# Kernel optimization log

Measured on AMD Instinct MI355X. Metric: run time of the kernel, lower is better.

The kernel has to match this reference:

```python
import jax, jax.numpy as jnp
import numpy as np


def pairwise_distance(x):
    # x: [B,N,F] -> squared euclidean distance matrix [B,N,N]
    sq = jnp.sum(x * x, axis=-1)
    d = sq[:, :, None] + sq[:, None, :] - 2.0 * jnp.einsum('bnd,bmd->bnm', x, x)
    return jnp.maximum(d, 0.0)


def knn_adjacency(dist, k):
    # keep the k nearest neighbors of each point (binary adjacency)
    B, N, _ = dist.shape
    idx = jax.lax.top_k(-dist, k)[1]  # [B,N,k]
    A = jnp.zeros((B, N, N), dist.dtype)
    return A.at[jnp.arange(B)[:, None, None], jnp.arange(N)[None, :, None], idx].set(1.0)


def get_laplacian(A):
    # normalized graph Laplacian L = I - D^{-1/2} A D^{-1/2}
    d = jnp.sum(A, axis=-1)
    dinv = jnp.where(d > 0, 1.0 / jnp.sqrt(jnp.maximum(d, 1e-12)), 0.0)
    An = A * dinv[:, :, None] * dinv[:, None, :]
    return jnp.eye(A.shape[-1], dtype=A.dtype)[None] - An


def cheb_conv(x, L, W, b, K):
    # DenseChebConv: Chebyshev recurrence T0=x, T1=Lx, Tk=2L T_{k-1}-T_{k-2};
    # concat along features then dense projection. x:[B,N,Fin], W:[K*Fin,Fout]
    xs = [x]
    if K > 1:
        xs.append(jnp.einsum('bnm,bmf->bnf', L, x))
    for _ in range(2, K):
        xs.append(2.0 * jnp.einsum('bnm,bmf->bnf', L, xs[-1]) - xs[-2])
    xk = jnp.concatenate(xs, axis=-1)
    return jnp.einsum('bnf,fo->bno', xk, W) + b


def segment_max(out, idx):
    # fused replacement of the per-batch/per-cluster python loops:
    # out:[B,N,F], idx:[B,R,S] -> max-pooled cluster features [B,R,F]
    B = out.shape[0]
    g = out[jnp.arange(B)[:, None, None], idx]  # [B,R,S,F]
    return jnp.max(g, axis=2)


def setup_inputs():
    key = jax.random.key(0)
    ks = jax.random.split(key, 12)
    B, N, R, S, P = 32, 1024, 64, 16, 55
    inp = {}
    inp['x'] = jax.random.normal(ks[0], (B, N, 7), jnp.float32)
    inp['x2'] = jax.random.normal(ks[1], (B, N, 3), jnp.float32)
    inp['laplacian_Reeb'] = jax.random.normal(ks[2], (B, R, R), jnp.float32)
    inp['W1'] = jax.random.normal(ks[3], (3 * 7, 64), jnp.float32) * 0.1
    inp['b1'] = jnp.zeros((64,), jnp.float32)
    inp['W_reeb'] = jax.random.normal(ks[4], (6 * 64, 256), jnp.float32) * 0.05
    inp['b_reeb'] = jnp.zeros((256,), jnp.float32)
    inp['W_fps'] = jax.random.normal(ks[5], (6 * 64, 256), jnp.float32) * 0.05
    inp['b_fps'] = jnp.zeros((256,), jnp.float32)
    inp['fc1_w'] = jax.random.normal(ks[6], (512, 256), jnp.float32) * 0.05
    inp['fc1_b'] = jnp.zeros((256,), jnp.float32)
    inp['fc3_w'] = jax.random.normal(ks[7], (256, 40), jnp.float32) * 0.05
    inp['fc3_b'] = jnp.zeros((40,), jnp.float32)
    inp['sccs'] = jax.random.randint(ks[8], (B, R, S), 0, N)
    inp['sccs_fps'] = jax.random.randint(ks[9], (B, P, N), 0, N)
    inp['k'] = 30
    inp['batch_size'] = B
    inp['num_points'] = N
    return inp


def reference(x, x2, laplacian_Reeb, W1, b1, W_reeb, b_reeb, W_fps, b_fps,
              fc1_w, fc1_b, fc3_w, fc3_b, sccs, sccs_fps, k, batch_size, num_points):
    sg = jax.lax.stop_gradient
    # point-cloud kNN Laplacian (torch.no_grad in original)
    L = sg(get_laplacian(knn_adjacency(pairwise_distance(x), k)))
    out = jax.nn.relu(cheb_conv(x, L, W1, b1, 3))  # [B,N,64]
    reg1 = jnp.sum(jnp.einsum('bnf,bnm,bmg->bfg', out, L, out) ** 2)
    # Reeb-graph segment max pooling (no_grad in original)
    V_reeb = sg(segment_max(out, sccs))  # [B,R,64]
    L_reeb = sg(laplacian_Reeb)
    out_reeb = jax.nn.relu(cheb_conv(V_reeb, L_reeb, W_reeb, b_reeb, 6))  # [B,R,256]
    reg2 = jnp.sum(jnp.einsum('bnf,bnm,bmg->bfg', out_reeb, L_reeb, out_reeb) ** 2)
    # FPS cluster max pooling (no_grad in original)
    V_fps = sg(segment_max(out, sccs_fps))  # [B,55,64]
    L_fps = sg(get_laplacian(pairwise_distance(V_fps)))
    out_fps = jax.nn.relu(cheb_conv(V_fps, L_fps, W_fps, b_fps, 6))  # [B,55,256]
    reg3 = jnp.sum(jnp.einsum('bnf,bnm,bmg->bfg', out_fps, L_fps, out_fps) ** 2)
    feat = jnp.concatenate([jnp.max(out_reeb, axis=1), jnp.max(out_fps, axis=1)], axis=1)  # [B,512]
    h = jax.nn.relu(feat @ fc1_w + fc1_b)
    logits = h @ fc3_w + fc3_b  # [B,40]
    regs = jnp.stack([reg1, reg2, reg3,
                      jnp.sum(fc1_w[:, 0] ** 2), fc1_b[0] ** 2,
                      jnp.sum(fc3_w[:, 0] ** 2), fc3_b[0] ** 2])
    return logits, regs
```

## Files before the change

### kernel.cpp

```cpp
#include <hip/hip_runtime.h>
#include <math.h>

#define BN 32
#define NP 1024
#define KNN 30
#define NR 64
#define NFPS 55

#define XSLOT(r) ((r) * 8 + ((r) >> 7) * 4)

__device__ __forceinline__ float lap_s() {
    const float dv = 1.0f / sqrtf(30.0f);
    return dv * dv;
}

__device__ __forceinline__ float dist7(const float4& xiA, const float4& xiB,
                                       float sqi, const float4& ca, const float4& cb) {
#pragma clang fp contract(off)
    float dot = xiA.x * ca.x;
    dot = fmaf(xiA.y, ca.y, dot);
    dot = fmaf(xiA.z, ca.z, dot);
    dot = fmaf(xiA.w, ca.w, dot);
    dot = fmaf(xiB.x, cb.x, dot);
    dot = fmaf(xiB.y, cb.y, dot);
    dot = fmaf(xiB.z, cb.z, dot);
    float r = sqi + cb.w;
    r = r - 2.f * dot;
    return fmaxf(r, 0.f);
}

__global__ __launch_bounds__(256, 4) void k_knn(const float* __restrict__ x,
                                                int* __restrict__ knn,
                                                float* __restrict__ xs1) {
    __shared__ float xls[8224];
    int b = blockIdx.x;
    int t = threadIdx.x;
    int ln = t & 63, wv = t >> 6;
    int seg = ln & 7;
    int rl  = ln >> 3;

    const float* xb = x + (size_t)b * NP * 7;
#pragma unroll 4
    for (int k = 0; k < 32; ++k) {
        int q = k * 256 + t;
        int r = q >> 3, d = q & 7;
        float v = (d < 7) ? xb[r * 7 + d] : 0.f;
        float p2 = v * v;
        p2 += __shfl_xor(p2, 1);
        p2 += __shfl_xor(p2, 2);
        p2 += __shfl_xor(p2, 4);
        xls[XSLOT(r) + d] = (d < 7) ? v : p2;
    }
    __syncthreads();

    int grow = blockIdx.y * 32 + wv * 8 + rl;
    int gslot = XSLOT(grow);
    float4 xiA = *(const float4*)&xls[gslot];
    float4 xiB = *(const float4*)&xls[gslot + 4];
    float sqi = xiB.w;

    float bd[KNN];
#pragma unroll
    for (int q = 0; q < KNN; ++q) bd[q] = __builtin_inff();
    int jbase = seg * 128;
    int sbase = XSLOT(jbase);
    for (int jc = 0; jc < 128; jc += 4) {
        const float* p = &xls[sbase + jc * 8];
        float4 a0 = *(const float4*)(p +  0), b0 = *(const float4*)(p +  4);
        float4 a1 = *(const float4*)(p +  8), b1 = *(const float4*)(p + 12);
        float4 a2 = *(const float4*)(p + 16), b2 = *(const float4*)(p + 20);
        float4 a3 = *(const float4*)(p + 24), b3 = *(const float4*)(p + 28);
        float d0 = dist7(xiA, xiB, sqi, a0, b0);
        float d1 = dist7(xiA, xiB, sqi, a1, b1);
        float d2 = dist7(xiA, xiB, sqi, a2, b2);
        float d3 = dist7(xiA, xiB, sqi, a3, b3);
#pragma unroll
        for (int q = KNN - 1; q >= 1; --q) bd[q] = __builtin_amdgcn_fmed3f(bd[q - 1], d0, bd[q]);
        bd[0] = fminf(bd[0], d0);
#pragma unroll
        for (int q = KNN - 1; q >= 1; --q) bd[q] = __builtin_amdgcn_fmed3f(bd[q - 1], d1, bd[q]);
        bd[0] = fminf(bd[0], d1);
#pragma unroll
        for (int q = KNN - 1; q >= 1; --q) bd[q] = __builtin_amdgcn_fmed3f(bd[q - 1], d2, bd[q]);
        bd[0] = fminf(bd[0], d2);
#pragma unroll
        for (int q = KNN - 1; q >= 1; --q) bd[q] = __builtin_amdgcn_fmed3f(bd[q - 1], d3, bd[q]);
        bd[0] = fminf(bd[0], d3);
    }

    float m[32];
#pragma unroll
    for (int q = 0; q < KNN; ++q) m[q] = bd[q];
    m[30] = __builtin_inff(); m[31] = __builtin_inff();
#pragma unroll
    for (int lvl = 0; lvl < 3; ++lvl) {
        int mask = 1 << lvl;
#pragma unroll
        for (int q = 0; q < 16; ++q) {
            float u = __shfl_xor(m[31 - q], mask);
            float v = __shfl_xor(m[q], mask);
            float lo = fminf(m[q], u);
            float hi = fminf(m[31 - q], v);
            m[q] = lo; m[31 - q] = hi;
        }
#pragma unroll
        for (int d = 16; d >= 1; d >>= 1) {
#pragma unroll
            for (int i = 0; i < 32; ++i) {
                if ((i & d) == 0) {
                    float a = m[i], c = m[i | d];
                    m[i] = fminf(a, c);
                    m[i | d] = fmaxf(a, c);
                }
            }
        }
    }
    float T = m[29];
    int firstT = 0;
#pragma unroll
    for (int q = 0; q < KNN; ++q) firstT += (m[q] < T) ? 1 : 0;
    int need = KNN - firstT;
    int cnt_lt = 0, cnt_eq = 0;
#pragma unroll
    for (int q = 0; q < KNN; ++q) {
        cnt_lt += (bd[q] < T) ? 1 : 0;
        cnt_eq += (bd[q] == T) ? 1 : 0;
    }
    int lanebase = ln & ~7;
    int pe = 0;
#pragma unroll
    for (int s2 = 0; s2 < 7; ++s2) {
        int v = __shfl(cnt_eq, lanebase + s2);
        pe += (s2 < seg) ? v : 0;
    }
    int e = need - pe;
    e = (e < 0) ? 0 : e;
    e = (e > cnt_eq) ? cnt_eq : e;
    int tk = cnt_lt + e;
    int pb = 0;
#pragma unroll
    for (int s2 = 0; s2 < 7; ++s2) {
        int v = __shfl(tk, lanebase + s2);
        pb += (s2 < seg) ? v : 0;
    }
    int base = pb;

    int* kout = knn + ((size_t)b * NP + grow) * KNN;
    float n0 = 0.f, n1 = 0.f, n2 = 0.f, n3 = 0.f, n4 = 0.f, n5 = 0.f, n6 = 0.f;
    int cs = 0, ct = 0;
    for (int jc = 0; jc < 128; jc += 4) {
        const float* p = &xls[sbase + jc * 8];
        float4 a0 = *(const float4*)(p +  0), b0 = *(const float4*)(p +  4);
        float4 a1 = *(const float4*)(p +  8), b1 = *(const float4*)(p + 12);
        float4 a2 = *(const float4*)(p + 16), b2 = *(const float4*)(p + 20);
        float4 a3 = *(const float4*)(p + 24), b3 = *(const float4*)(p + 28);
        float d0 = dist7(xiA, xiB, sqi, a0, b0);
        float d1 = dist7(xiA, xiB, sqi, a1, b1);
        float d2 = dist7(xiA, xiB, sqi, a2, b2);
        float d3 = dist7(xiA, xiB, sqi, a3, b3);
#pragma unroll
        for (int u = 0; u < 4; ++u) {
            float dist = (u == 0) ? d0 : (u == 1) ? d1 : (u == 2) ? d2 : d3;
            const float4& ca = (u == 0) ? a0 : (u == 1) ? a1 : (u == 2) ? a2 : a3;
            const float4& cb = (u == 0) ? b0 : (u == 1) ? b1 : (u == 2) ? b2 : b3;
            bool lt = dist < T;
            bool eq = (dist == T) && (ct < e);
            if ((lt || eq) && (cs + ct < tk)) {
                kout[base + cs + ct] = jbase + jc + u;
                cs += lt ? 1 : 0;
                ct += eq ? 1 : 0;
                n0 += ca.x; n1 += ca.y; n2 += ca.z; n3 += ca.w;
                n4 += cb.x; n5 += cb.y; n6 += cb.z;
            }
        }
    }
    for (int q = cs + ct; q < tk; ++q) kout[base + q] = grow;
#pragma unroll
    for (int mask = 1; mask <= 4; mask <<= 1) {
        n0 += __shfl_xor(n0, mask);
        n1 += __shfl_xor(n1, mask);
        n2 += __shfl_xor(n2, mask);
        n3 += __shfl_xor(n3, mask);
        n4 += __shfl_xor(n4, mask);
        n5 += __shfl_xor(n5, mask);
        n6 += __shfl_xor(n6, mask);
    }
    if (seg < 7) {
        float nv = (seg == 0) ? n0 : (seg == 1) ? n1 : (seg == 2) ? n2 :
                   (seg == 3) ? n3 : (seg == 4) ? n4 : (seg == 5) ? n5 : n6;
        xs1[((size_t)b * NP + grow) * 7 + seg] = xls[gslot + seg] - lap_s() * nv;
    }
}

__global__ __launch_bounds__(256) void k_out(const float* __restrict__ x,
                                             const float* __restrict__ xs1,
                                             const int* __restrict__ knn,
                                             const float* __restrict__ W1,
                                             const float* __restrict__ b1,
                                             float* __restrict__ out,
                                             const float* __restrict__ fc1_w,
                                             const float* __restrict__ fc1_b,
                                             const float* __restrict__ fc3_w,
                                             const float* __restrict__ fc3_b,
                                             float* __restrict__ regs,
                                             float* __restrict__ Cbuf) {
    __shared__ float x1s[NP * 7];
    __shared__ float x0s[64 * 7];
    __shared__ float fr[64 * 21];
    __shared__ float W1s[21 * 64];
    __shared__ float b1s[64];
    __shared__ float nsp[64 * 28];
    int b = blockIdx.x, y = blockIdx.y;
    int t = threadIdx.x;
    if (y == 16) {
        float* cb = Cbuf + (size_t)b * 4096;
        for (int q = t; q < 4096; q += 256) cb[q] = 0.f;
        if (b != 0) return;
        float* r1 = x1s;
        float* r2 = x1s + 256;
        float s1 = 0.f;
        for (int i = t; i < 512; i += 256) { float v = fc1_w[(size_t)i * 256]; s1 += v * v; }
        float v2 = fc3_w[(size_t)t * 40];
        r1[t] = s1; r2[t] = v2 * v2;
        __syncthreads();
        for (int st = 128; st > 0; st >>= 1) {
            if (t < st) { r1[t] += r1[t + st]; r2[t] += r2[t + st]; }
            __syncthreads();
        }
        if (t == 0) {
            regs[0] = 0.f; regs[1] = 0.f; regs[2] = 0.f;
            regs[3] = r1[0];
            regs[4] = fc1_b[0] * fc1_b[0];
            regs[5] = r2[0];
            regs[6] = fc3_b[0] * fc3_b[0];
        }
        return;
    }
    int rbase = y * 64;
    for (int q = t; q < NP * 7; q += 256) x1s[q] = xs1[(size_t)b * NP * 7 + q];
    for (int q = t; q < 64 * 7; q += 256) x0s[q] = x[(size_t)b * NP * 7 + (size_t)rbase * 7 + q];
    for (int q = t; q < 21 * 64; q += 256) W1s[q] = W1[q];
    if (t < 64) b1s[t] = b1[t];
    __syncthreads();
    {
        int row = t >> 2, tq = t & 3;
        int i = rbase + row;
        float ns[7] = {0.f, 0.f, 0.f, 0.f, 0.f, 0.f, 0.f};
        const int* kn = knn + ((size_t)b * NP + i) * KNN;
        for (int q = tq; q < KNN; q += 4) {
            int j = kn[q];
#pragma unroll
            for (int d = 0; d < 7; ++d) ns[d] += x1s[j * 7 + d];
        }
#pragma unroll
        for (int d = 0; d < 7; ++d) nsp[row * 28 + tq * 7 + d] = ns[d];
    }
    __syncthreads();
    if (t < 64) {
        int i = rbase + t;
        float f[21];
#pragma unroll
        for (int d = 0; d < 7; ++d) { f[d] = x0s[t * 7 + d]; f[7 + d] = x1s[i * 7 + d]; }
        const float s = lap_s();
#pragma unroll
        for (int d = 0; d < 7; ++d) {
            float ns = nsp[t * 28 + d] + nsp[t * 28 + 7 + d]
                     + nsp[t * 28 + 14 + d] + nsp[t * 28 + 21 + d];
            f[14 + d] = 2.f * (f[7 + d] - s * ns) - f[d];
        }
#pragma unroll
        for (int d = 0; d < 21; ++d) fr[t * 21 + d] = f[d];
    }
    __syncthreads();
    int o = t & 63, g = t >> 6;
    for (int m = 0; m < 16; ++m) {
        int r = g * 16 + m;
        float acc = b1s[o];
#pragma unroll
        for (int d = 0; d < 21; ++d) acc += fr[r * 21 + d] * W1s[d * 64 + o];
        out[((size_t)b * NP + rbase + r) * 64 + o] = fmaxf(acc, 0.f);
    }
}

__global__ __launch_bounds__(256) void k_z1v(const float* __restrict__ out,
                                             const int* __restrict__ knn,
                                             const int* __restrict__ sccs,
                                             const int* __restrict__ sccs_fps,
                                             float* __restrict__ Z1,
                                             float* __restrict__ Vr,
                                             float* __restrict__ Vf) {
    __shared__ unsigned bmw[32];
    __shared__ float red[256];
    int b = blockIdx.x, y = blockIdx.y;
    int t = threadIdx.x;
    const float* ob = out + (size_t)b * NP * 64;
    if (y < 256) {
        int i = y * 4 + (t >> 6);
        int f = t & 63;
        const int* kn = knn + ((size_t)b * NP + i) * KNN;
        float sum = 0.f;
        for (int q = 0; q < KNN; ++q) sum += ob[(size_t)kn[q] * 64 + f];
        Z1[((size_t)b * NP + i) * 64 + f] = ob[(size_t)i * 64 + f] - lap_s() * sum;
    } else if (y < 272) {
        int r = (y - 256) * 4 + (t >> 6);
        int f = t & 63;
        const int* sc = sccs + ((size_t)b * NR + r) * 16;
        float m = -__builtin_inff();
        for (int q = 0; q < 16; ++q) m = fmaxf(m, ob[(size_t)sc[q] * 64 + f]);
        Vr[((size_t)b * NR + r) * 64 + f] = m;
    } else {
        int p = y - 272;
        const int* sp = sccs_fps + ((size_t)b * NFPS + p) * 1024;
        if (t < 32) bmw[t] = 0u;
        __syncthreads();
        for (int q = t; q < 1024; q += 256) {
            int r = sp[q];
            atomicOr(&bmw[r >> 5], 1u << (r & 31));
        }
        __syncthreads();
        int f = t & 63, sc = t >> 6;
        float m = -__builtin_inff();
        for (int w0 = sc * 8; w0 < sc * 8 + 8; ++w0) {
            unsigned w = bmw[w0];
            while (w) {
                int bit = __ffs(w) - 1;
                w &= w - 1;
                m = fmaxf(m, ob[(size_t)(w0 * 32 + bit) * 64 + f]);
            }
        }
        red[t] = m; __syncthreads();
        if (sc == 0) {
            m = fmaxf(fmaxf(red[f], red[64 + f]), fmaxf(red[128 + f], red[192 + f]));
            Vf[((size_t)b * NFPS + p) * 64 + f] = m;
        }
    }
}

__device__ __forceinline__ void t1_part(const float* __restrict__ out,
                                        const float* __restrict__ Z1,
                                        float* __restrict__ Cbuf,
                                        float* buf, int y) {
    int b = blockIdx.x, t = threadIdx.x;
    float* os = buf;
    float* zs = buf + 8192;
    const float* ob = out + ((size_t)b * NP + (size_t)y * 128) * 64;
    const float* zb = Z1 + ((size_t)b * NP + (size_t)y * 128) * 64;
    for (int q = t; q < 128 * 64; q += 256) { os[q] = ob[q]; zs[q] = zb[q]; }
    __syncthreads();
    int f0 = (t & 15) * 4, g0 = (t >> 4) * 4;
    float4 ac0 = make_float4(0.f, 0.f, 0.f, 0.f);
    float4 ac1 = ac0, ac2 = ac0, ac3 = ac0;
#pragma unroll 4
    for (int n = 0; n < 128; ++n) {
        float4 ov = *(const float4*)&os[n * 64 + f0];
        float4 zv = *(const float4*)&zs[n * 64 + g0];
        ac0.x += ov.x * zv.x; ac0.y += ov.x * zv.y; ac0.z += ov.x * zv.z; ac0.w += ov.x * zv.w;
        ac1.x += ov.y * zv.x; ac1.y += ov.y * zv.y; ac1.z += ov.y * zv.z; ac1.w += ov.y * zv.w;
        ac2.x += ov.z * zv.x; ac2.y += ov.z * zv.y; ac2.z += ov.z * zv.z; ac2.w += ov.z * zv.w;
        ac3.x += ov.w * zv.x; ac3.y += ov.w * zv.y; ac3.z += ov.w * zv.z; ac3.w += ov.w * zv.w;
    }
    float* cb = Cbuf + (size_t)b * 4096;
    atomicAdd(&cb[(f0 + 0) * 64 + g0 + 0], ac0.x);
    atomicAdd(&cb[(f0 + 0) * 64 + g0 + 1], ac0.y);
    atomicAdd(&cb[(f0 + 0) * 64 + g0 + 2], ac0.z);
    atomicAdd(&cb[(f0 + 0) * 64 + g0 + 3], ac0.w);
    atomicAdd(&cb[(f0 + 1) * 64 + g0 + 0], ac1.x);
    atomicAdd(&cb[(f0 + 1) * 64 + g0 + 1], ac1.y);
    atomicAdd(&cb[(f0 + 1) * 64 + g0 + 2], ac1.z);
    atomicAdd(&cb[(f0 + 1) * 64 + g0 + 3], ac1.w);
    atomicAdd(&cb[(f0 + 2) * 64 + g0 + 0], ac2.x);
    atomicAdd(&cb[(f0 + 2) * 64 + g0 + 1], ac2.y);
    atomicAdd(&cb[(f0 + 2) * 64 + g0 + 2], ac2.z);
    atomicAdd(&cb[(f0 + 2) * 64 + g0 + 3], ac2.w);
    atomicAdd(&cb[(f0 + 3) * 64 + g0 + 0], ac3.x);
    atomicAdd(&cb[(f0 + 3) * 64 + g0 + 1], ac3.y);
    atomicAdd(&cb[(f0 + 3) * 64 + g0 + 2], ac3.z);
    atomicAdd(&cb[(f0 + 3) * 64 + g0 + 3], ac3.w);
}

__device__ __forceinline__ void lfps_impl(const float* __restrict__ Vfps,
                                          float* __restrict__ Lf, float* buf) {
    int b = blockIdx.x;
    int t = threadIdx.x;
    float* Vs = buf;
    float* sq = buf + 3520;
    float* dist = buf + 3584;
    float* dinv = buf + 6609;
    for (int q = t; q < NFPS * 64; q += 256) Vs[q] = Vfps[(size_t)b * NFPS * 64 + q];
    __syncthreads();
    if (t < NFPS) {
        float s = 0.f;
        for (int f = 0; f < 64; ++f) { float v = Vs[t * 64 + f]; s += v * v; }
        sq[t] = s;
    }
    __syncthreads();
    for (int q = t; q < NFPS * NFPS; q += 256) {
        int i = q / NFPS, j = q % NFPS;
        float dot = 0.f;
        for (int f = 0; f < 64; ++f) dot += Vs[i * 64 + f] * Vs[j * 64 + f];
        dist[q] = fmaxf(sq[i] + sq[j] - 2.f * dot, 0.f);
    }
    __syncthreads();
    if (t < NFPS) {
        float s = 0.f;
        for (int j = 0; j < NFPS; ++j) s += dist[t * NFPS + j];
        dinv[t] = (s > 0.f) ? 1.0f / sqrtf(fmaxf(s, 1e-12f)) : 0.f;
    }
    __syncthreads();
    for (int q = t; q < NFPS * NFPS; q += 256) {
        int i = q / NFPS, j = q % NFPS;
        Lf[(size_t)b * NFPS * NFPS + q] = ((i == j) ? 1.f : 0.f) - dist[q] * dinv[i] * dinv[j];
    }
}

template<int N>
__device__ __forceinline__ void cheb_impl(const float* __restrict__ L,
                                          const float* __restrict__ V,
                                          const float* __restrict__ W,
                                          const float* __restrict__ bias,
                                          float* __restrict__ out,
                                          float* __restrict__ Z,
                                          float* Ls, float* bA, float* bB, float* Ws,
                                          int b, int sl) {
    constexpr int NPAD = (N + 3) & ~3;
    int t = threadIdx.x;
    int c0 = (t & 15) * 4;
    int r0 = (t >> 4) * 4;

    for (int q = t; q < 64 * 64; q += 256) { Ls[q] = 0.f; bA[q] = 0.f; bB[q] = 0.f; }
    __syncthreads();
    for (int q = t; q < N * N; q += 256) {
        int r = q / N, m = q % N;
        Ls[r * 64 + m] = L[(size_t)b * N * N + q];
    }
    for (int q = t; q < N * 64; q += 256) bA[q] = V[(size_t)b * N * 64 + q];
    {
        const float* Wk = W + sl * 64;
        for (int q = t; q < 64 * 64; q += 256) Ws[q] = Wk[(q >> 6) * 256 + (q & 63)];
    }
    float4 a4[4];
    {
        float4 bv = *(const float4*)&bias[sl * 64 + c0];
#pragma unroll
        for (int i = 0; i < 4; ++i) a4[i] = bv;
    }
    __syncthreads();

    auto accum = [&](const float* xb) {
#pragma unroll 2
        for (int m = 0; m < 64; m += 4) {
            float4 xv[4], wv[4];
#pragma unroll
            for (int i = 0; i < 4; ++i) xv[i] = *(const float4*)&xb[(r0 + i) * 64 + m];
#pragma unroll
            for (int mm = 0; mm < 4; ++mm) wv[mm] = *(const float4*)&Ws[(m + mm) * 64 + c0];
#pragma unroll
            for (int i = 0; i < 4; ++i) {
                float xi0 = xv[i].x, xi1 = xv[i].y, xi2 = xv[i].z, xi3 = xv[i].w;
                a4[i].x += xi0 * wv[0].x; a4[i].y += xi0 * wv[0].y; a4[i].z += xi0 * wv[0].z; a4[i].w += xi0 * wv[0].w;
                a4[i].x += xi1 * wv[1].x; a4[i].y += xi1 * wv[1].y; a4[i].z += xi1 * wv[1].z; a4[i].w += xi1 * wv[1].w;
                a4[i].x += xi2 * wv[2].x; a4[i].y += xi2 * wv[2].y; a4[i].z += xi2 * wv[2].z; a4[i].w += xi2 * wv[2].w;
                a4[i].x += xi3 * wv[3].x; a4[i].y += xi3 * wv[3].y; a4[i].z += xi3 * wv[3].z; a4[i].w += xi3 * wv[3].w;
            }
        }
    };
    auto chebmm = [&](const float* src, float* dst, bool first) {
        float4 acc[4];
#pragma unroll
        for (int i = 0; i < 4; ++i) acc[i] = make_float4(0.f, 0.f, 0.f, 0.f);
#pragma unroll 2
        for (int m = 0; m < NPAD; m += 4) {
            float4 sv[4], lv[4];
#pragma unroll
            for (int mm = 0; mm < 4; ++mm) sv[mm] = *(const float4*)&src[(m + mm) * 64 + c0];
#pragma unroll
            for (int i = 0; i < 4; ++i) lv[i] = *(const float4*)&Ls[(r0 + i) * 64 + m];
#pragma unroll
            for (int i = 0; i < 4; ++i) {
                float l0 = lv[i].x, l1 = lv[i].y, l2 = lv[i].z, l3 = lv[i].w;
                acc[i].x += l0 * sv[0].x; acc[i].y += l0 * sv[0].y; acc[i].z += l0 * sv[0].z; acc[i].w += l0 * sv[0].w;
                acc[i].x += l1 * sv[1].x; acc[i].y += l1 * sv[1].y; acc[i].z += l1 * sv[1].z; acc[i].w += l1 * sv[1].w;
                acc[i].x += l2 * sv[2].x; acc[i].y += l2 * sv[2].y; acc[i].z += l2 * sv[2].z; acc[i].w += l2 * sv[2].w;
                acc[i].x += l3 * sv[3].x; acc[i].y += l3 * sv[3].y; acc[i].z += l3 * sv[3].z; acc[i].w += l3 * sv[3].w;
            }
        }
#pragma unroll
        for (int i = 0; i < 4; ++i) {
            if (r0 + i < N) {
                float4* d = (float4*)&dst[(r0 + i) * 64 + c0];
                if (first) *d = acc[i];
                else {
                    float4 od = *d;
                    *d = make_float4(2.f * acc[i].x - od.x, 2.f * acc[i].y - od.y,
                                     2.f * acc[i].z - od.z, 2.f * acc[i].w - od.w);
                }
            }
        }
    };
    auto loadW = [&](int k) {
        const float* Wk = W + (size_t)k * 64 * 256 + sl * 64;
        for (int q = t; q < 64 * 64; q += 256) Ws[q] = Wk[(q >> 6) * 256 + (q & 63)];
    };

    accum(bA);                 __syncthreads();
    chebmm(bA, bB, true);      loadW(1);  __syncthreads();
    accum(bB);                 __syncthreads();
    chebmm(bB, bA, false);     loadW(2);  __syncthreads();
    accum(bA);                 __syncthreads();
    chebmm(bA, bB, false);     loadW(3);  __syncthreads();
    accum(bB);                 __syncthreads();
    chebmm(bB, bA, false);     loadW(4);  __syncthreads();
    accum(bA);                 __syncthreads();
    chebmm(bA, bB, false);     loadW(5);  __syncthreads();
    accum(bB);                 __syncthreads();

    float* ob = out + (size_t)b * N * 256 + sl * 64;
#pragma unroll
    for (int i = 0; i < 4; ++i) {
        if (r0 + i < N) {
            float4 v = make_float4(fmaxf(a4[i].x, 0.f), fmaxf(a4[i].y, 0.f),
                                   fmaxf(a4[i].z, 0.f), fmaxf(a4[i].w, 0.f));
            *(float4*)&bA[(r0 + i) * 64 + c0] = v;
            *(float4*)&ob[(size_t)(r0 + i) * 256 + c0] = v;
        }
    }
    __syncthreads();
    {
        float4 acc[4];
#pragma unroll
        for (int i = 0; i < 4; ++i) acc[i] = make_float4(0.f, 0.f, 0.f, 0.f);
#pragma unroll 2
        for (int m = 0; m < NPAD; m += 4) {
            float4 sv[4], lv[4];
#pragma unroll
            for (int mm = 0; mm < 4; ++mm) sv[mm] = *(const float4*)&bA[(m + mm) * 64 + c0];
#pragma unroll
            for (int i = 0; i < 4; ++i) lv[i] = *(const float4*)&Ls[(r0 + i) * 64 + m];
#pragma unroll
            for (int i = 0; i < 4; ++i) {
                float l0 = lv[i].x, l1 = lv[i].y, l2 = lv[i].z, l3 = lv[i].w;
                acc[i].x += l0 * sv[0].x; acc[i].y += l0 * sv[0].y; acc[i].z += l0 * sv[0].z; acc[i].w += l0 * sv[0].w;
                acc[i].x += l1 * sv[1].x; acc[i].y += l1 * sv[1].y; acc[i].z += l1 * sv[1].z; acc[i].w += l1 * sv[1].w;
                acc[i].x += l2 * sv[2].x; acc[i].y += l2 * sv[2].y; acc[i].z += l2 * sv[2].z; acc[i].w += l2 * sv[2].w;
                acc[i].x += l3 * sv[3].x; acc[i].y += l3 * sv[3].y; acc[i].z += l3 * sv[3].z; acc[i].w += l3 * sv[3].w;
            }
        }
        float* zb = Z + (size_t)b * N * 256 + sl * 64;
#pragma unroll
        for (int i = 0; i < 4; ++i)
            if (r0 + i < N) *(float4*)&zb[(size_t)(r0 + i) * 256 + c0] = acc[i];
    }
}

template<int N>
__device__ __forceinline__ void treg_impl(const float* __restrict__ out,
                                          const float* __restrict__ Z,
                                          float* __restrict__ reg,
                                          float* zs, float* os, float* red, int y) {
    int b = blockIdx.x;
    int f0 = (y >> 1) * 32;
    int g0 = (y & 1) * 128;
    int t = threadIdx.x;
    for (int q = t; q < N * 128; q += 256) {
        int r = q >> 7, gl = q & 127;
        zs[q] = Z[(size_t)b * N * 256 + r * 256 + g0 + gl];
    }
    for (int q = t; q < N * 32; q += 256) {
        int r = q >> 5, f = q & 31;
        os[q] = out[(size_t)b * N * 256 + r * 256 + f0 + f];
    }
    __syncthreads();
    int fl = t >> 3;
    int gb = (t & 7) * 16;
    float accv[16];
#pragma unroll
    for (int q = 0; q < 16; ++q) accv[q] = 0.f;
    for (int n = 0; n < N; ++n) {
        float a = os[n * 32 + fl];
        const float* zr = zs + n * 128 + gb;
#pragma unroll
        for (int q = 0; q < 16; ++q) accv[q] += a * zr[q];
    }
    float loc = 0.f;
#pragma unroll
    for (int q = 0; q < 16; ++q) loc += accv[q] * accv[q];
    red[t] = loc; __syncthreads();
    for (int st = 128; st > 0; st >>= 1) { if (t < st) red[t] += red[t + st]; __syncthreads(); }
    if (t == 0) atomicAdd(reg, red[0]);
}

__global__ __launch_bounds__(256) void k_mid1(
        const float* __restrict__ out, const float* __restrict__ Z1,
        const float* __restrict__ Vfps, float* __restrict__ Cbuf,
        float* __restrict__ Lf,
        const float* __restrict__ Lr, const float* __restrict__ Vr,
        const float* __restrict__ Wr, const float* __restrict__ br,
        float* __restrict__ outR, float* __restrict__ Zr) {
    __shared__ float smem[16384];
    int y = blockIdx.y;
    if (y < 8)       t1_part(out, Z1, Cbuf, smem, y);
    else if (y == 8) lfps_impl(Vfps, Lf, smem);
    else cheb_impl<NR>(Lr, Vr, Wr, br, outR, Zr,
                       smem, smem + 4096, smem + 8192, smem + 12288,
                       blockIdx.x, y - 9);
}

__global__ __launch_bounds__(256) void k_mid2(
        const float* __restrict__ Lf, const float* __restrict__ Vf,
        const float* __restrict__ Wf, const float* __restrict__ bf,
        float* __restrict__ outP, float* __restrict__ Zf,
        const float* __restrict__ outR, const float* __restrict__ Zr,
        const float* __restrict__ Cbuf, float* __restrict__ regs) {
    __shared__ float smem[16384];
    int y = blockIdx.y;
    if (y < 4) cheb_impl<NFPS>(Lf, Vf, Wf, bf, outP, Zf,
                               smem, smem + 4096, smem + 8192, smem + 12288,
                               blockIdx.x, y);
    else if (y < 20) treg_impl<NR>(outR, Zr, regs + 1, smem, smem + 8192, smem + 10240, y - 4);
    else {
        int b = blockIdx.x, t = threadIdx.x;
        float* red = smem;
        float loc = 0.f;
        for (int q = t; q < 4096; q += 256) { float v = Cbuf[(size_t)b * 4096 + q]; loc += v * v; }
        red[t] = loc; __syncthreads();
        for (int st = 128; st > 0; st >>= 1) { if (t < st) red[t] += red[t + st]; __syncthreads(); }
        if (t == 0) atomicAdd(&regs[0], red[0]);
    }
}

__global__ __launch_bounds__(256) void k_fin(
        const float* __restrict__ outP, const float* __restrict__ Zf,
        const float* __restrict__ outR,
        const float* __restrict__ fc1_w, const float* __restrict__ fc1_b,
        const float* __restrict__ fc3_w, const float* __restrict__ fc3_b,
        float* __restrict__ regs, float* __restrict__ logits) {
    __shared__ float smem[10496];
    int y = blockIdx.y;
    if (y < 16) treg_impl<NFPS>(outP, Zf, regs + 2, smem, smem + 8192, smem + 10240, y);
    else {
        int b = blockIdx.x, t = threadIdx.x;
        float* feat = smem;
        float* h = smem + 8192;
        float m = -__builtin_inff();
        for (int r = 0; r < NR; ++r) m = fmaxf(m, outR[((size_t)b * NR + r) * 256 + t]);
        feat[t] = m;
        m = -__builtin_inff();
        for (int p = 0; p < NFPS; ++p) m = fmaxf(m, outP[((size_t)b * NFPS + p) * 256 + t]);
        feat[256 + t] = m;
        __syncthreads();
        float a = fc1_b[t];
        for (int i = 0; i < 512; ++i) a += feat[i] * fc1_w[(size_t)i * 256 + t];
        h[t] = fmaxf(a, 0.f);
        __syncthreads();
        if (t < 40) {
            float a2 = fc3_b[t];
            for (int i = 0; i < 256; ++i) a2 += h[i] * fc3_w[(size_t)i * 40 + t];
            logits[(size_t)b * 40 + t] = a2;
        }
    }
}

extern "C" void kernel_launch(void* const* d_in, const int* in_sizes, int n_in,
                              void* d_out, int out_size, void* d_ws, size_t ws_size,
                              hipStream_t stream) {
    const float* x      = (const float*)d_in[0];
    const float* L_reeb = (const float*)d_in[2];
    const float* W1     = (const float*)d_in[3];
    const float* b1     = (const float*)d_in[4];
    const float* W_reeb = (const float*)d_in[5];
    const float* b_reeb = (const float*)d_in[6];
    const float* W_fps  = (const float*)d_in[7];
    const float* b_fps  = (const float*)d_in[8];
    const float* fc1_w  = (const float*)d_in[9];
    const float* fc1_b  = (const float*)d_in[10];
    const float* fc3_w  = (const float*)d_in[11];
    const float* fc3_b  = (const float*)d_in[12];
    const int*   sccs   = (const int*)d_in[13];
    const int*   sccs_f = (const int*)d_in[14];

    float* outv = (float*)d_out;
    float* regs = outv + 1280;

    char* w = (char*)d_ws;
    size_t off = 0;
    auto alloc = [&](size_t bytes) { void* p = w + off; off = (off + bytes + 255) & ~(size_t)255; return p; };
    int*   knn   = (int*)  alloc((size_t)BN * NP * KNN * 4);
    float* xs1   = (float*)alloc((size_t)BN * NP * 7 * 4);
    float* outF  = (float*)alloc((size_t)BN * NP * 64 * 4);
    float* Z1    = (float*)alloc((size_t)BN * NP * 64 * 4);
    float* Vreeb = (float*)alloc((size_t)BN * NR * 64 * 4);
    float* outRb = (float*)alloc((size_t)BN * NR * 256 * 4);
    float* Z2    = (float*)alloc((size_t)BN * NR * 256 * 4);
    float* Vfps  = (float*)alloc((size_t)BN * NFPS * 64 * 4);
    float* Lfps  = (float*)alloc((size_t)BN * NFPS * NFPS * 4);
    float* outP  = (float*)alloc((size_t)BN * NFPS * 256 * 4);
    float* Z3    = (float*)alloc((size_t)BN * NFPS * 256 * 4);
    float* Cbuf  = (float*)alloc((size_t)BN * 4096 * 4);

    k_knn<<<dim3(BN, NP / 32), 256, 0, stream>>>(x, knn, xs1);
    k_out<<<dim3(BN, 17), 256, 0, stream>>>(x, xs1, knn, W1, b1, outF,
                                            fc1_w, fc1_b, fc3_w, fc3_b, regs, Cbuf);
    k_z1v<<<dim3(BN, 256 + 16 + NFPS), 256, 0, stream>>>(outF, knn, sccs, sccs_f,
                                                         Z1, Vreeb, Vfps);
    k_mid1<<<dim3(BN, 13), 256, 0, stream>>>(outF, Z1, Vfps, Cbuf, Lfps,
                                             L_reeb, Vreeb, W_reeb, b_reeb, outRb, Z2);
    k_mid2<<<dim3(BN, 21), 256, 0, stream>>>(Lfps, Vfps, W_fps, b_fps, outP, Z3,
                                             outRb, Z2, Cbuf, regs);
    k_fin<<<dim3(BN, 17), 256, 0, stream>>>(outP, Z3, outRb,
                                            fc1_w, fc1_b, fc3_w, fc3_b, regs, outv);
}
```

Before: 356.0 us.

## Compute Chebyshev regularizers via N-by-N Gram matrix identity

The regularizer sum((O^T L O)^2) is now computed as sum((O O^T) ⊙ (Z Z^T)), where Z = L O. This forms two small N×N Gram matrices over the 256 features instead of a 256×256 feature-by-feature product. Because N is 64 or 55, each batch needs far fewer FLOPs and fits in one block, so the grids of k_mid2 and k_fin shrink. The cost is less block-level parallelism for this stage and a different floating-point summation order.

```diff
diff --git a/kernel.cpp b/kernel.cpp
--- a/kernel.cpp
+++ b/kernel.cpp
@@ -553,37 +553,63 @@
 }
 
 template<int N>
-__device__ __forceinline__ void treg_impl(const float* __restrict__ out,
-                                          const float* __restrict__ Z,
+__device__ __forceinline__ void gram_impl(const float* __restrict__ Ob,
+                                          const float* __restrict__ Zb,
                                           float* __restrict__ reg,
-                                          float* zs, float* os, float* red, int y) {
-    int b = blockIdx.x;
-    int f0 = (y >> 1) * 32;
-    int g0 = (y & 1) * 128;
-    int t = threadIdx.x;
-    for (int q = t; q < N * 128; q += 256) {
-        int r = q >> 7, gl = q & 127;
-        zs[q] = Z[(size_t)b * N * 256 + r * 256 + g0 + gl];
-    }
-    for (int q = t; q < N * 32; q += 256) {
-        int r = q >> 5, f = q & 31;
-        os[q] = out[(size_t)b * N * 256 + r * 256 + f0 + f];
-    }
-    __syncthreads();
-    int fl = t >> 3;
-    int gb = (t & 7) * 16;
-    float accv[16];
-#pragma unroll
-    for (int q = 0; q < 16; ++q) accv[q] = 0.f;
-    for (int n = 0; n < N; ++n) {
-        float a = os[n * 32 + fl];
-        const float* zr = zs + n * 128 + gb;
-#pragma unroll
-        for (int q = 0; q < 16; ++q) accv[q] += a * zr[q];
+                                          float* buf) {
+    int b = blockIdx.x, t = threadIdx.x;
+    float* os = buf;
+    float* zs = buf + 4352;
+    float* red = buf + 8704;
+    int n0 = (t >> 4) * 4, m0 = (t & 15) * 4;
+    float a1[4][4], a2[4][4];
+#pragma unroll
+    for (int i = 0; i < 4; ++i)
+#pragma unroll
+        for (int j = 0; j < 4; ++j) { a1[i][j] = 0.f; a2[i][j] = 0.f; }
+    for (int fc = 0; fc < 4; ++fc) {
+        for (int q = t; q < 64 * 64; q += 256) {
+            int n = q >> 6, f = q & 63;
+            float vo = 0.f, vz = 0.f;
+            if (n < N) {
+                size_t idx = ((size_t)b * N + n) * 256 + fc * 64 + f;
+                vo = Ob[idx];
+                vz = Zb[idx];
+            }
+            os[n * 68 + f] = vo;
+            zs[n * 68 + f] = vz;
+        }
+        __syncthreads();
+#pragma unroll 2
+        for (int f = 0; f < 64; f += 4) {
+            float4 oa[4], obv[4], za[4], zbv[4];
+#pragma unroll
+            for (int i = 0; i < 4; ++i) {
+                oa[i] = *(const float4*)&os[(n0 + i) * 68 + f];
+                za[i] = *(const float4*)&zs[(n0 + i) * 68 + f];
+            }
+#pragma unroll
+            for (int j = 0; j < 4; ++j) {
+                obv[j] = *(const float4*)&os[(m0 + j) * 68 + f];
+                zbv[j] = *(const float4*)&zs[(m0 + j) * 68 + f];
+            }
+#pragma unroll
+            for (int i = 0; i < 4; ++i)
+#pragma unroll
+                for (int j = 0; j < 4; ++j) {
+                    a1[i][j] += oa[i].x * obv[j].x + oa[i].y * obv[j].y
+                              + oa[i].z * obv[j].z + oa[i].w * obv[j].w;
+                    a2[i][j] += za[i].x * zbv[j].x + za[i].y * zbv[j].y
+                              + za[i].z * zbv[j].z + za[i].w * zbv[j].w;
+                }
+        }
+        __syncthreads();
     }
     float loc = 0.f;
 #pragma unroll
-    for (int q = 0; q < 16; ++q) loc += accv[q] * accv[q];
+    for (int i = 0; i < 4; ++i)
+#pragma unroll
+        for (int j = 0; j < 4; ++j) loc += a1[i][j] * a2[i][j];
     red[t] = loc; __syncthreads();
     for (int st = 128; st > 0; st >>= 1) { if (t < st) red[t] += red[t + st]; __syncthreads(); }
     if (t == 0) atomicAdd(reg, red[0]);
@@ -616,7 +642,7 @@
     if (y < 4) cheb_impl<NFPS>(Lf, Vf, Wf, bf, outP, Zf,
                                smem, smem + 4096, smem + 8192, smem + 12288,
                                blockIdx.x, y);
-    else if (y < 20) treg_impl<NR>(outR, Zr, regs + 1, smem, smem + 8192, smem + 10240, y - 4);
+    else if (y == 4) gram_impl<NR>(outR, Zr, regs + 1, smem);
     else {
         int b = blockIdx.x, t = threadIdx.x;
         float* red = smem;
@@ -634,13 +660,13 @@
         const float* __restrict__ fc1_w, const float* __restrict__ fc1_b,
         const float* __restrict__ fc3_w, const float* __restrict__ fc3_b,
         float* __restrict__ regs, float* __restrict__ logits) {
-    __shared__ float smem[10496];
+    __shared__ float smem[8960];
     int y = blockIdx.y;
-    if (y < 16) treg_impl<NFPS>(outP, Zf, regs + 2, smem, smem + 8192, smem + 10240, y);
+    if (y == 0) gram_impl<NFPS>(outP, Zf, regs + 2, smem);
     else {
         int b = blockIdx.x, t = threadIdx.x;
         float* feat = smem;
-        float* h = smem + 8192;
+        float* h = smem + 1024;
         float m = -__builtin_inff();
         for (int r = 0; r < NR; ++r) m = fmaxf(m, outR[((size_t)b * NR + r) * 256 + t]);
         feat[t] = m;
@@ -704,8 +730,8 @@
                                                          Z1, Vreeb, Vfps);
     k_mid1<<<dim3(BN, 13), 256, 0, stream>>>(outF, Z1, Vfps, Cbuf, Lfps,
                                              L_reeb, Vreeb, W_reeb, b_reeb, outRb, Z2);
-    k_mid2<<<dim3(BN, 21), 256, 0, stream>>>(Lfps, Vfps, W_fps, b_fps, outP, Z3,
-                                             outRb, Z2, Cbuf, regs);
-    k_fin<<<dim3(BN, 17), 256, 0, stream>>>(outP, Z3, outRb,
-                                            fc1_w, fc1_b, fc3_w, fc3_b, regs, outv);
-}
+    k_mid2<<<dim3(BN, 6), 256, 0, stream>>>(Lfps, Vfps, W_fps, b_fps, outP, Z3,
+                                            outRb, Z2, Cbuf, regs);
+    k_fin<<<dim3(BN, 2), 256, 0, stream>>>(outP, Z3, outRb,
+                                           fc1_w, fc1_b, fc3_w, fc3_b, regs, outv);
+}
```

New measurement: 365.9 us. +2.8%, slower.

## Regroup mid-stage kernels so both Chebyshev convs and all regularizers share launches

Applied to the files above, without the earlier changes.

Reorganizes the three trailing launches. The first runs the T1 partials and the FPS Laplacian, the second runs the Reeb and FPS Chebyshev convolutions together, and the last runs both regularizer reductions, the Cbuf reduction and the FC head. This balances work per launch and shortens the dependency chain so the two independent Chebyshev stages run concurrently. The launch count stays the same, but the final kernel now mixes heavier treg blocks with the head blocks.

```diff
diff --git a/kernel.cpp b/kernel.cpp
--- a/kernel.cpp
+++ b/kernel.cpp
@@ -589,35 +589,45 @@
     if (t == 0) atomicAdd(reg, red[0]);
 }
 
-__global__ __launch_bounds__(256) void k_mid1(
+__global__ __launch_bounds__(256) void k_midA(
         const float* __restrict__ out, const float* __restrict__ Z1,
         const float* __restrict__ Vfps, float* __restrict__ Cbuf,
-        float* __restrict__ Lf,
+        float* __restrict__ Lf) {
+    __shared__ float smem[16384];
+    int y = blockIdx.y;
+    if (y < 8) t1_part(out, Z1, Cbuf, smem, y);
+    else       lfps_impl(Vfps, Lf, smem);
+}
+
+__global__ __launch_bounds__(256) void k_midB(
         const float* __restrict__ Lr, const float* __restrict__ Vr,
         const float* __restrict__ Wr, const float* __restrict__ br,
-        float* __restrict__ outR, float* __restrict__ Zr) {
+        float* __restrict__ outR, float* __restrict__ Zr,
+        const float* __restrict__ Lf, const float* __restrict__ Vf,
+        const float* __restrict__ Wf, const float* __restrict__ bf,
+        float* __restrict__ outP, float* __restrict__ Zf) {
     __shared__ float smem[16384];
     int y = blockIdx.y;
-    if (y < 8)       t1_part(out, Z1, Cbuf, smem, y);
-    else if (y == 8) lfps_impl(Vfps, Lf, smem);
-    else cheb_impl<NR>(Lr, Vr, Wr, br, outR, Zr,
-                       smem, smem + 4096, smem + 8192, smem + 12288,
-                       blockIdx.x, y - 9);
-}
-
-__global__ __launch_bounds__(256) void k_mid2(
-        const float* __restrict__ Lf, const float* __restrict__ Vf,
-        const float* __restrict__ Wf, const float* __restrict__ bf,
-        float* __restrict__ outP, float* __restrict__ Zf,
+    if (y < 4) cheb_impl<NR>(Lr, Vr, Wr, br, outR, Zr,
+                             smem, smem + 4096, smem + 8192, smem + 12288,
+                             blockIdx.x, y);
+    else       cheb_impl<NFPS>(Lf, Vf, Wf, bf, outP, Zf,
+                               smem, smem + 4096, smem + 8192, smem + 12288,
+                               blockIdx.x, y - 4);
+}
+
+__global__ __launch_bounds__(256) void k_fin(
         const float* __restrict__ outR, const float* __restrict__ Zr,
-        const float* __restrict__ Cbuf, float* __restrict__ regs) {
-    __shared__ float smem[16384];
+        const float* __restrict__ outP, const float* __restrict__ Zf,
+        const float* __restrict__ Cbuf,
+        const float* __restrict__ fc1_w, const float* __restrict__ fc1_b,
+        const float* __restrict__ fc3_w, const float* __restrict__ fc3_b,
+        float* __restrict__ regs, float* __restrict__ logits) {
+    __shared__ float smem[10496];
     int y = blockIdx.y;
-    if (y < 4) cheb_impl<NFPS>(Lf, Vf, Wf, bf, outP, Zf,
-                               smem, smem + 4096, smem + 8192, smem + 12288,
-                               blockIdx.x, y);
-    else if (y < 20) treg_impl<NR>(outR, Zr, regs + 1, smem, smem + 8192, smem + 10240, y - 4);
-    else {
+    if (y < 16) treg_impl<NR>(outR, Zr, regs + 1, smem, smem + 8192, smem + 10240, y);
+    else if (y < 32) treg_impl<NFPS>(outP, Zf, regs + 2, smem, smem + 8192, smem + 10240, y - 16);
+    else if (y == 32) {
         int b = blockIdx.x, t = threadIdx.x;
         float* red = smem;
         float loc = 0.f;
@@ -625,22 +635,10 @@
         red[t] = loc; __syncthreads();
         for (int st = 128; st > 0; st >>= 1) { if (t < st) red[t] += red[t + st]; __syncthreads(); }
         if (t == 0) atomicAdd(&regs[0], red[0]);
-    }
-}
-
-__global__ __launch_bounds__(256) void k_fin(
-        const float* __restrict__ outP, const float* __restrict__ Zf,
-        const float* __restrict__ outR,
-        const float* __restrict__ fc1_w, const float* __restrict__ fc1_b,
-        const float* __restrict__ fc3_w, const float* __restrict__ fc3_b,
-        float* __restrict__ regs, float* __restrict__ logits) {
-    __shared__ float smem[10496];
-    int y = blockIdx.y;
-    if (y < 16) treg_impl<NFPS>(outP, Zf, regs + 2, smem, smem + 8192, smem + 10240, y);
-    else {
+    } else {
         int b = blockIdx.x, t = threadIdx.x;
         float* feat = smem;
-        float* h = smem + 8192;
+        float* h = smem + 1024;
         float m = -__builtin_inff();
         for (int r = 0; r < NR; ++r) m = fmaxf(m, outR[((size_t)b * NR + r) * 256 + t]);
         feat[t] = m;
@@ -702,10 +700,9 @@
                                             fc1_w, fc1_b, fc3_w, fc3_b, regs, Cbuf);
     k_z1v<<<dim3(BN, 256 + 16 + NFPS), 256, 0, stream>>>(outF, knn, sccs, sccs_f,
                                                          Z1, Vreeb, Vfps);
-    k_mid1<<<dim3(BN, 13), 256, 0, stream>>>(outF, Z1, Vfps, Cbuf, Lfps,
-                                             L_reeb, Vreeb, W_reeb, b_reeb, outRb, Z2);
-    k_mid2<<<dim3(BN, 21), 256, 0, stream>>>(Lfps, Vfps, W_fps, b_fps, outP, Z3,
-                                             outRb, Z2, Cbuf, regs);
-    k_fin<<<dim3(BN, 17), 256, 0, stream>>>(outP, Z3, outRb,
+    k_midA<<<dim3(BN, 9), 256, 0, stream>>>(outF, Z1, Vfps, Cbuf, Lfps);
+    k_midB<<<dim3(BN, 8), 256, 0, stream>>>(L_reeb, Vreeb, W_reeb, b_reeb, outRb, Z2,
+                                            Lfps, Vfps, W_fps, b_fps, outP, Z3);
+    k_fin<<<dim3(BN, 34), 256, 0, stream>>>(outRb, Z2, outP, Z3, Cbuf,
                                             fc1_w, fc1_b, fc3_w, fc3_b, regs, outv);
 }
```

Result: slower. 366.3 us (+2.9%).
